# Kernel optimization log

Hardware: AMD Instinct MI355X
Metric: run time of the kernel (lower is better)

Reference implementation:

```python
import jax, jax.numpy as jnp
import numpy as np

EPS = 1e-9  # Dice BatchNormalization epsilon


def dice(x, alpha):
    # Keras BatchNormalization(axis=-1, center=False, scale=False) in training
    # mode: normalize over all axes except the last using batch statistics.
    mean = jnp.mean(x, axis=(0, 1), keepdims=True)
    var = jnp.var(x, axis=(0, 1), keepdims=True)
    x_normed = (x - mean) * jax.lax.rsqrt(var + EPS)
    p = jax.nn.sigmoid(x_normed)
    return alpha * (1.0 - p) * x + p * x


def setup_inputs() -> dict:
    key = jax.random.key(0)
    ks = jax.random.split(key, 11)
    B, T, D = 512, 2048, 20
    keys_ = jax.random.normal(ks[0], (B, T, D), dtype=jnp.float32)
    query = jax.random.normal(ks[1], (B, 1, D), dtype=jnp.float32)
    mask = jax.random.randint(ks[2], (B, T), 0, 2) > 0
    # DNN tower weights: hidden dims 80 -> 32 -> 16, attention head 16 -> 1
    W0 = jax.random.normal(ks[3], (80, 32), dtype=jnp.float32) * 0.1
    b0 = jax.random.normal(ks[4], (32,), dtype=jnp.float32) * 0.1
    a0 = jax.random.normal(ks[5], (32,), dtype=jnp.float32) * 0.1
    W1 = jax.random.normal(ks[6], (32, 16), dtype=jnp.float32) * 0.1
    b1 = jax.random.normal(ks[7], (16,), dtype=jnp.float32) * 0.1
    a1 = jax.random.normal(ks[8], (16,), dtype=jnp.float32) * 0.1
    wk = jax.random.normal(ks[9], (16, 1), dtype=jnp.float32) * 0.1
    bk = jax.random.normal(ks[10], (1,), dtype=jnp.float32) * 0.1
    return {"keys": keys_, "query": query, "mask": mask,
            "W0": W0, "b0": b0, "a0": a0,
            "W1": W1, "b1": b1, "a1": a1,
            "wk": wk, "bk": bk}


def reference(keys, query, mask, W0, b0, a0, W1, b1, a1, wk, bk):
    B, T, D = keys.shape
    # repeat query along the key/time axis: [B,1,D] -> [B,T,D]
    queries = jnp.broadcast_to(query, (B, T, D))
    # local-activation features: [B,T,4D] = [B,T,80]
    att = jnp.concatenate([queries, keys, queries - keys, queries * keys], axis=-1)
    # DNN tower with Dice activations (dropout is identity at inference)
    h = dice(att @ W0 + b0, a0)   # [B,T,32]
    h = dice(h @ W1 + b1, a1)     # [B,T,16]
    score = h @ wk + bk           # [B,T,1]
    outputs = jnp.transpose(score, (0, 2, 1))  # [B,1,T]
    # NOTE: the original code computes the masked scores into self.outputs but
    # then (weight_normalization=False, return_score=False) overwrites it with
    # matmul(outputs, keys) using the UNMASKED scores -- we reproduce that.
    return jnp.matmul(outputs, keys)  # [B,1,D]
```

## Files before the change

kernel.cpp:

```cpp
#include <hip/hip_runtime.h>
#include <hip/hip_cooperative_groups.h>

namespace cg = cooperative_groups;


#define BB 512
#define TT 2048
#define DD 20
#define C0 32
#define C1 16

#define NTH 256
#define NPOS 2
#define POSB (NTH * NPOS)
#define CHUNK 1024
#define NROUND (CHUNK / POSB)
#define NBLK (TT / CHUNK)
#define GRID (BB * NBLK)
#define NSLOT 8

#define WS_P1 0
#define WS_P2 512
#define WS_ZERO_N 768
#define WS_BLOB 896
#define BLOB_J 24
#define BLOB_B (C0 * BLOB_J)

#define PIN(x) asm volatile("" : "+v"(x))
#define AGLOAD(p) \
    __hip_atomic_load((p), __ATOMIC_RELAXED, __HIP_MEMORY_SCOPE_AGENT)

__device__ __forceinline__ float fast_sigmoid(float x) {
    return __builtin_amdgcn_rcpf(1.0f + __expf(-x));
}

__device__ __forceinline__ void load_krow(const float* __restrict__ row,
                                          float* kk) {
    const float4* kr = (const float4*)row;
    float4 a = kr[0], b = kr[1], c = kr[2], d = kr[3], e = kr[4];
    kk[0] = a.x; kk[1] = a.y; kk[2] = a.z; kk[3] = a.w;
    kk[4] = b.x; kk[5] = b.y; kk[6] = b.z; kk[7] = b.w;
    kk[8] = c.x; kk[9] = c.y; kk[10] = c.z; kk[11] = c.w;
    kk[12] = d.x; kk[13] = d.y; kk[14] = d.z; kk[15] = d.w;
    kk[16] = e.x; kk[17] = e.y; kk[18] = e.z; kk[19] = e.w;
}

__global__ void prep_kernel(const float* __restrict__ query,
                            const float* __restrict__ W0,
                            const float* __restrict__ b0,
                            float* __restrict__ blob, float* __restrict__ ws,
                            float* __restrict__ out) {
    const int b = blockIdx.x * 2 + (threadIdx.x >> 5);
    const int j = threadIdx.x & 31;
    if (blockIdx.x == 0) {
        for (int i = threadIdx.x; i < WS_ZERO_N; i += 64) ws[i] = 0.f;
    }
    if (j < DD) out[b * DD + j] = 0.f;
    float cj = b0[j];
    float* dst = blob + (size_t)b * BLOB_B + j * BLOB_J;
#pragma unroll
    for (int d = 0; d < DD; ++d) {
        float w_q = W0[d * C0 + j];
        float w_k = W0[(DD + d) * C0 + j];
        float w_d = W0[(2 * DD + d) * C0 + j];
        float w_p = W0[(3 * DD + d) * C0 + j];
        float qd = query[b * DD + d];
        dst[d] = w_k - w_d + qd * w_p;
        cj = fmaf(qd, w_q + w_d, cj);
    }
    dst[20] = cj;
}

#define LOAD_AND_PIN_KEYS(r)                                                 \
    float kk[NPOS][DD];                                                      \
    _Pragma("unroll") for (int pp = 0; pp < NPOS; ++pp)                      \
        load_krow(kbase + (size_t)((r)*POSB + tid + pp * NTH) * DD, kk[pp]); \
    _Pragma("unroll") for (int pp = 0; pp < NPOS; ++pp)                      \
        _Pragma("unroll") for (int d = 0; d < DD; ++d) PIN(kk[pp][d]);

#define TOWER_JLOOP()                                                        \
    _Pragma("unroll 1") for (int j = 0; j < C0; ++j) {                       \
        const float* wr = bA + j * BLOB_J;                                   \
        const float* ur = W1 + j * C1;                                       \
        const float cj = wr[20];                                             \
        const float2 ss = lss0[j];                                           \
        const float al = a0[j];                                              \
        const float nal = 1.0f - al;                                         \
        float h[NPOS];                                                       \
        _Pragma("unroll") for (int pp = 0; pp < NPOS; ++pp) {                \
            float hh = cj;                                                   \
            _Pragma("unroll") for (int d = 0; d < DD; ++d)                   \
                hh = fmaf(kk[pp][d], wr[d], hh);                             \
            h[pp] = hh;                                                      \
        }                                                                    \
        _Pragma("unroll") for (int pp = 0; pp < NPOS; ++pp) {                \
            float pr = fast_sigmoid(fmaf(h[pp], ss.x, ss.y));                \
            float h0d = h[pp] * fmaf(pr, nal, al);                           \
            _Pragma("unroll") for (int c = 0; c < C1; ++c)                   \
                h1[pp][c] = fmaf(h0d, ur[c], h1[pp][c]);                     \
        }                                                                    \
    }

__device__ __forceinline__ void phase1_body(int slot, int tid, int lane,
                                            const float* __restrict__ bA,
                                            const float* __restrict__ kbase,
                                            float* __restrict__ ws) {
    float s[C0], q[C0];
#pragma unroll
    for (int j = 0; j < C0; ++j) { s[j] = 0.f; q[j] = 0.f; }
#pragma unroll 1
    for (int r = 0; r < NROUND; ++r) {
        LOAD_AND_PIN_KEYS(r)
#pragma unroll
        for (int j = 0; j < C0; ++j) {
            const float* wr = bA + j * BLOB_J;
            const float cj = wr[20];
            float sv = 0.f, qv = 0.f;
#pragma unroll
            for (int pp = 0; pp < NPOS; ++pp) {
                float hh = cj;
#pragma unroll
                for (int d = 0; d < DD; ++d) hh = fmaf(kk[pp][d], wr[d], hh);
                sv += hh;
                qv = fmaf(hh, hh, qv);
            }
            s[j] += sv;
            q[j] += qv;
        }
    }
    float redv = 0.f;
#pragma unroll
    for (int v = 0; v < 2 * C0; ++v) {
        float val = (v < C0) ? s[v] : q[v - C0];
#pragma unroll
        for (int o = 32; o >= 1; o >>= 1) val += __shfl_xor(val, o);
        if (lane == v) redv = val;
    }
    atomicAdd(&ws[WS_P1 + slot * (2 * C0) + lane], redv);
}

__device__ __forceinline__ void finalize0(int tid, float* __restrict__ ws,
                                          float2* __restrict__ lss0) {
    if (tid < C0) {
        float sv = 0.f, qv = 0.f;
#pragma unroll
        for (int k = 0; k < NSLOT; ++k) {
            sv += AGLOAD(&ws[WS_P1 + k * (2 * C0) + tid]);
            qv += AGLOAD(&ws[WS_P1 + k * (2 * C0) + C0 + tid]);
        }
        const float invN = 1.0f / (float)(BB * TT);
        float mean = sv * invN;
        float var = qv * invN - mean * mean;
        float sc = rsqrtf(var + 1e-9f);
        lss0[tid] = make_float2(sc, -mean * sc);
    }
}

__device__ __forceinline__ void phase2_body(
    int slot, int tid, int lane, const float* __restrict__ bA,
    const float* __restrict__ kbase, const float* __restrict__ a0,
    const float* __restrict__ W1, const float* __restrict__ b1,
    const float2* __restrict__ lss0, float* __restrict__ ws) {
    float s1[C1], q1[C1];
#pragma unroll
    for (int c = 0; c < C1; ++c) { s1[c] = 0.f; q1[c] = 0.f; }
#pragma unroll 1
    for (int r = 0; r < NROUND; ++r) {
        LOAD_AND_PIN_KEYS(r)
        float h1[NPOS][C1];
#pragma unroll
        for (int pp = 0; pp < NPOS; ++pp)
#pragma unroll
            for (int c = 0; c < C1; ++c) h1[pp][c] = 0.f;
        TOWER_JLOOP()
#pragma unroll
        for (int c = 0; c < C1; ++c) {
            float bc = b1[c];
#pragma unroll
            for (int pp = 0; pp < NPOS; ++pp) {
                float v = h1[pp][c] + bc;
                s1[c] += v;
                q1[c] = fmaf(v, v, q1[c]);
            }
        }
    }
    float redv = 0.f;
#pragma unroll
    for (int v = 0; v < 2 * C1; ++v) {
        float val = (v < C1) ? s1[v] : q1[v - C1];
#pragma unroll
        for (int o = 32; o >= 1; o >>= 1) val += __shfl_xor(val, o);
        if (lane == v) redv = val;
    }
    if (lane < 2 * C1)
        atomicAdd(&ws[WS_P2 + slot * (2 * C1) + lane], redv);
}

__device__ __forceinline__ void finalize1(int tid, float* __restrict__ ws,
                                          const float* __restrict__ a1,
                                          const float* __restrict__ wk,
                                          float4* __restrict__ ld1v) {
    if (tid < C1) {
        float sv = 0.f, qv = 0.f;
#pragma unroll
        for (int k = 0; k < NSLOT; ++k) {
            sv += AGLOAD(&ws[WS_P2 + k * (2 * C1) + tid]);
            qv += AGLOAD(&ws[WS_P2 + k * (2 * C1) + C1 + tid]);
        }
        const float invN = 1.0f / (float)(BB * TT);
        float mean = sv * invN;
        float var = qv * invN - mean * mean;
        float sc = rsqrtf(var + 1e-9f);
        ld1v[tid] = make_float4(sc, -mean * sc, a1[tid], wk[tid]);
    }
}

__device__ __forceinline__ void phase3_body(
    int batch, int tid, int lane, int wave, const float* __restrict__ bA,
    const float* __restrict__ kbase, const float* __restrict__ a0,
    const float* __restrict__ W1, const float* __restrict__ b1,
    const float* __restrict__ bk, const float2* __restrict__ lss0,
    const float4* __restrict__ ld1v, float (*red)[DD],
    float* __restrict__ out) {
    const float bkv = bk[0];
    float oacc[DD];
#pragma unroll
    for (int d = 0; d < DD; ++d) oacc[d] = 0.f;
#pragma unroll 1
    for (int r = 0; r < NROUND; ++r) {
        LOAD_AND_PIN_KEYS(r)
        float h1[NPOS][C1];
#pragma unroll
        for (int pp = 0; pp < NPOS; ++pp)
#pragma unroll
            for (int c = 0; c < C1; ++c) h1[pp][c] = 0.f;
        TOWER_JLOOP()
#pragma unroll
        for (int pp = 0; pp < NPOS; ++pp) {
            float score = bkv;
#pragma unroll
            for (int c = 0; c < C1; ++c) {
                float v = h1[pp][c] + b1[c];
                float4 dv = ld1v[c];
                float pr = fast_sigmoid(fmaf(v, dv.x, dv.y));
                float hd = v * fmaf(pr, 1.0f - dv.z, dv.z);
                score = fmaf(hd, dv.w, score);
            }
#pragma unroll
            for (int d = 0; d < DD; ++d)
                oacc[d] = fmaf(score, kk[pp][d], oacc[d]);
        }
    }
    float redv = 0.f;
#pragma unroll
    for (int v = 0; v < DD; ++v) {
        float val = oacc[v];
#pragma unroll
        for (int o = 32; o >= 1; o >>= 1) val += __shfl_xor(val, o);
        if (lane == v) redv = val;
    }
    if (lane < DD) red[wave][lane] = redv;
    __syncthreads();
    if (tid < DD)
        atomicAdd(&out[batch * DD + tid],
                  red[0][tid] + red[1][tid] + red[2][tid] + red[3][tid]);
}

__global__ __launch_bounds__(NTH, 2) void fused_kernel(
    const float* __restrict__ keys, const float* __restrict__ blob,
    const float* __restrict__ a0, const float* __restrict__ W1,
    const float* __restrict__ b1, const float* __restrict__ a1,
    const float* __restrict__ wk, const float* __restrict__ bk,
    float* __restrict__ ws, float* __restrict__ out) {
    const int batch = blockIdx.x >> 1, chunk = blockIdx.x & 1;
    const int slot = blockIdx.x & (NSLOT - 1);
    const int tid = threadIdx.x, wave = tid >> 6, lane = tid & 63;
    const float* bA = blob + (size_t)batch * BLOB_B;
    const float* kbase = keys + ((size_t)batch * TT + chunk * CHUNK) * DD;

    __shared__ float2 lss0[C0];
    __shared__ float4 ld1v[C1];
    __shared__ float red[4][DD];

    phase1_body(slot, tid, lane, bA, kbase, ws);
    cg::this_grid().sync();
    finalize0(tid, ws, lss0);
    __syncthreads();
    phase2_body(slot, tid, lane, bA, kbase, a0, W1, b1, lss0, ws);
    cg::this_grid().sync();
    finalize1(tid, ws, a1, wk, ld1v);
    __syncthreads();
    phase3_body(batch, tid, lane, wave, bA, kbase, a0, W1, b1, bk, lss0,
                ld1v, red, out);
}

__global__ __launch_bounds__(NTH, 2) void pass1_kernel(
    const float* __restrict__ keys, const float* __restrict__ blob,
    float* __restrict__ ws) {
    const int batch = blockIdx.x >> 1, chunk = blockIdx.x & 1;
    const int tid = threadIdx.x, lane = tid & 63;
    phase1_body(blockIdx.x & (NSLOT - 1), tid, lane,
                blob + (size_t)batch * BLOB_B,
                keys + ((size_t)batch * TT + chunk * CHUNK) * DD, ws);
}

__global__ __launch_bounds__(NTH, 2) void pass2_kernel(
    const float* __restrict__ keys, const float* __restrict__ blob,
    const float* __restrict__ a0, const float* __restrict__ W1,
    const float* __restrict__ b1, float* __restrict__ ws) {
    const int batch = blockIdx.x >> 1, chunk = blockIdx.x & 1;
    const int tid = threadIdx.x, lane = tid & 63;
    __shared__ float2 lss0[C0];
    finalize0(tid, ws, lss0);
    __syncthreads();
    phase2_body(blockIdx.x & (NSLOT - 1), tid, lane,
                blob + (size_t)batch * BLOB_B,
                keys + ((size_t)batch * TT + chunk * CHUNK) * DD, a0, W1, b1,
                lss0, ws);
}

__global__ __launch_bounds__(NTH, 2) void pass3_kernel(
    const float* __restrict__ keys, const float* __restrict__ blob,
    const float* __restrict__ a0, const float* __restrict__ W1,
    const float* __restrict__ b1, const float* __restrict__ a1,
    const float* __restrict__ wk, const float* __restrict__ bk,
    float* __restrict__ ws, float* __restrict__ out) {
    const int batch = blockIdx.x >> 1, chunk = blockIdx.x & 1;
    const int tid = threadIdx.x, wave = tid >> 6, lane = tid & 63;
    __shared__ float2 lss0[C0];
    __shared__ float4 ld1v[C1];
    __shared__ float red[4][DD];
    finalize0(tid, ws, lss0);
    finalize1(tid, ws, a1, wk, ld1v);
    __syncthreads();
    phase3_body(batch, tid, lane, wave, blob + (size_t)batch * BLOB_B,
                keys + ((size_t)batch * TT + chunk * CHUNK) * DD, a0, W1, b1,
                bk, lss0, ld1v, red, out);
}

extern "C" void kernel_launch(void* const* d_in, const int* in_sizes, int n_in,
                              void* d_out, int out_size, void* d_ws,
                              size_t ws_size, hipStream_t stream) {
    const float* keys = (const float*)d_in[0];
    const float* query = (const float*)d_in[1];
    const float* W0 = (const float*)d_in[3];
    const float* b0 = (const float*)d_in[4];
    const float* a0 = (const float*)d_in[5];
    const float* W1 = (const float*)d_in[6];
    const float* b1 = (const float*)d_in[7];
    const float* a1 = (const float*)d_in[8];
    const float* wk = (const float*)d_in[9];
    const float* bk = (const float*)d_in[10];
    float* out = (float*)d_out;
    float* ws = (float*)d_ws;
    float* blob = ws + WS_BLOB;
    const float* blobc = blob;

    prep_kernel<<<BB / 2, 64, 0, stream>>>(query, W0, b0, blob, ws, out);

    static int use_coop = -1;
    if (use_coop < 0) {
        int nb = 0, ncu = 0;
        hipError_t e1 = hipOccupancyMaxActiveBlocksPerMultiprocessor(
            &nb, (const void*)fused_kernel, NTH, 0);
        hipDeviceProp_t prop;
        hipError_t e2 = hipGetDeviceProperties(&prop, 0);
        if (e2 == hipSuccess) ncu = prop.multiProcessorCount;
        use_coop = (e1 == hipSuccess && e2 == hipSuccess && nb * ncu >= GRID)
                       ? 1
                       : 0;
    }

    if (use_coop) {
        void* args[] = {(void*)&keys, (void*)&blobc, (void*)&a0, (void*)&W1,
                        (void*)&b1,   (void*)&a1,    (void*)&wk, (void*)&bk,
                        (void*)&ws,   (void*)&out};
        hipError_t e = hipLaunchCooperativeKernel(
            (const void*)fused_kernel, dim3(GRID), dim3(NTH), args, 0,
            stream);
        if (e != hipSuccess) use_coop = 0;
    }
    if (!use_coop) {
        pass1_kernel<<<GRID, NTH, 0, stream>>>(keys, blob, ws);
        pass2_kernel<<<GRID, NTH, 0, stream>>>(keys, blob, a0, W1, b1, ws);
        pass3_kernel<<<GRID, NTH, 0, stream>>>(keys, blob, a0, W1, b1, a1, wk,
                                               bk, ws, out);
    }
}
```

Baseline: 277.0 us.

## Stage key tiles through LDS with async double buffering, drop cooperative fused kernel

```diff
diff --git a/kernel.cpp b/kernel.cpp
--- a/kernel.cpp
+++ b/kernel.cpp
@@ -1,7 +1,4 @@
 #include <hip/hip_runtime.h>
-#include <hip/hip_cooperative_groups.h>
-
-namespace cg = cooperative_groups;
 
 
 #define BB 512
@@ -11,10 +8,9 @@
 #define C1 16
 
 #define NTH 256
-#define NPOS 2
-#define POSB (NTH * NPOS)
+#define TILE 256
 #define CHUNK 1024
-#define NROUND (CHUNK / POSB)
+#define SPB (CHUNK / TILE)
 #define NBLK (TT / CHUNK)
 #define GRID (BB * NBLK)
 #define NSLOT 8
@@ -30,14 +26,28 @@
 #define AGLOAD(p) \
     __hip_atomic_load((p), __ATOMIC_RELAXED, __HIP_MEMORY_SCOPE_AGENT)
 
+#define GAS __attribute__((address_space(1)))
+#define LAS __attribute__((address_space(3)))
+
 __device__ __forceinline__ float fast_sigmoid(float x) {
     return __builtin_amdgcn_rcpf(1.0f + __expf(-x));
 }
 
-__device__ __forceinline__ void load_krow(const float* __restrict__ row,
-                                          float* kk) {
-    const float4* kr = (const float4*)row;
-    float4 a = kr[0], b = kr[1], c = kr[2], d = kr[3], e = kr[4];
+__device__ __forceinline__ void stage_tile(const float* __restrict__ gsrc,
+                                           float* lbuf, int wave, int lane) {
+    const float* gw = gsrc + wave * 1280 + lane * 4;
+    float* lw_ = lbuf + wave * 1280;
+#pragma unroll
+    for (int u = 0; u < 5; ++u)
+        __builtin_amdgcn_global_load_lds((const GAS void*)(gw + u * 256),
+                                         (LAS void*)(lw_ + u * 256), 16, 0,
+                                         0);
+}
+
+__device__ __forceinline__ void load_row_lds(const float* __restrict__ row,
+                                             float* kk) {
+    const float4* r4 = (const float4*)row;
+    float4 a = r4[0], b = r4[1], c = r4[2], d = r4[3], e = r4[4];
     kk[0] = a.x; kk[1] = a.y; kk[2] = a.z; kk[3] = a.w;
     kk[4] = b.x; kk[5] = b.y; kk[6] = b.z; kk[7] = b.w;
     kk[8] = c.x; kk[9] = c.y; kk[10] = c.z; kk[11] = c.w;
@@ -71,74 +81,6 @@
     dst[20] = cj;
 }
 
-#define LOAD_AND_PIN_KEYS(r)                                                 \
-    float kk[NPOS][DD];                                                      \
-    _Pragma("unroll") for (int pp = 0; pp < NPOS; ++pp)                      \
-        load_krow(kbase + (size_t)((r)*POSB + tid + pp * NTH) * DD, kk[pp]); \
-    _Pragma("unroll") for (int pp = 0; pp < NPOS; ++pp)                      \
-        _Pragma("unroll") for (int d = 0; d < DD; ++d) PIN(kk[pp][d]);
-
-#define TOWER_JLOOP()                                                        \
-    _Pragma("unroll 1") for (int j = 0; j < C0; ++j) {                       \
-        const float* wr = bA + j * BLOB_J;                                   \
-        const float* ur = W1 + j * C1;                                       \
-        const float cj = wr[20];                                             \
-        const float2 ss = lss0[j];                                           \
-        const float al = a0[j];                                              \
-        const float nal = 1.0f - al;                                         \
-        float h[NPOS];                                                       \
-        _Pragma("unroll") for (int pp = 0; pp < NPOS; ++pp) {                \
-            float hh = cj;                                                   \
-            _Pragma("unroll") for (int d = 0; d < DD; ++d)                   \
-                hh = fmaf(kk[pp][d], wr[d], hh);                             \
-            h[pp] = hh;                                                      \
-        }                                                                    \
-        _Pragma("unroll") for (int pp = 0; pp < NPOS; ++pp) {                \
-            float pr = fast_sigmoid(fmaf(h[pp], ss.x, ss.y));                \
-            float h0d = h[pp] * fmaf(pr, nal, al);                           \
-            _Pragma("unroll") for (int c = 0; c < C1; ++c)                   \
-                h1[pp][c] = fmaf(h0d, ur[c], h1[pp][c]);                     \
-        }                                                                    \
-    }
-
-__device__ __forceinline__ void phase1_body(int slot, int tid, int lane,
-                                            const float* __restrict__ bA,
-                                            const float* __restrict__ kbase,
-                                            float* __restrict__ ws) {
-    float s[C0], q[C0];
-#pragma unroll
-    for (int j = 0; j < C0; ++j) { s[j] = 0.f; q[j] = 0.f; }
-#pragma unroll 1
-    for (int r = 0; r < NROUND; ++r) {
-        LOAD_AND_PIN_KEYS(r)
-#pragma unroll
-        for (int j = 0; j < C0; ++j) {
-            const float* wr = bA + j * BLOB_J;
-            const float cj = wr[20];
-            float sv = 0.f, qv = 0.f;
-#pragma unroll
-            for (int pp = 0; pp < NPOS; ++pp) {
-                float hh = cj;
-#pragma unroll
-                for (int d = 0; d < DD; ++d) hh = fmaf(kk[pp][d], wr[d], hh);
-                sv += hh;
-                qv = fmaf(hh, hh, qv);
-            }
-            s[j] += sv;
-            q[j] += qv;
-        }
-    }
-    float redv = 0.f;
-#pragma unroll
-    for (int v = 0; v < 2 * C0; ++v) {
-        float val = (v < C0) ? s[v] : q[v - C0];
-#pragma unroll
-        for (int o = 32; o >= 1; o >>= 1) val += __shfl_xor(val, o);
-        if (lane == v) redv = val;
-    }
-    atomicAdd(&ws[WS_P1 + slot * (2 * C0) + lane], redv);
-}
-
 __device__ __forceinline__ void finalize0(int tid, float* __restrict__ ws,
                                           float2* __restrict__ lss0) {
     if (tid < C0) {
@@ -154,46 +96,6 @@
         float sc = rsqrtf(var + 1e-9f);
         lss0[tid] = make_float2(sc, -mean * sc);
     }
-}
-
-__device__ __forceinline__ void phase2_body(
-    int slot, int tid, int lane, const float* __restrict__ bA,
-    const float* __restrict__ kbase, const float* __restrict__ a0,
-    const float* __restrict__ W1, const float* __restrict__ b1,
-    const float2* __restrict__ lss0, float* __restrict__ ws) {
-    float s1[C1], q1[C1];
-#pragma unroll
-    for (int c = 0; c < C1; ++c) { s1[c] = 0.f; q1[c] = 0.f; }
-#pragma unroll 1
-    for (int r = 0; r < NROUND; ++r) {
-        LOAD_AND_PIN_KEYS(r)
-        float h1[NPOS][C1];
-#pragma unroll
-        for (int pp = 0; pp < NPOS; ++pp)
-#pragma unroll
-            for (int c = 0; c < C1; ++c) h1[pp][c] = 0.f;
-        TOWER_JLOOP()
-#pragma unroll
-        for (int c = 0; c < C1; ++c) {
-            float bc = b1[c];
-#pragma unroll
-            for (int pp = 0; pp < NPOS; ++pp) {
-                float v = h1[pp][c] + bc;
-                s1[c] += v;
-                q1[c] = fmaf(v, v, q1[c]);
-            }
-        }
-    }
-    float redv = 0.f;
-#pragma unroll
-    for (int v = 0; v < 2 * C1; ++v) {
-        float val = (v < C1) ? s1[v] : q1[v - C1];
-#pragma unroll
-        for (int o = 32; o >= 1; o >>= 1) val += __shfl_xor(val, o);
-        if (lane == v) redv = val;
-    }
-    if (lane < 2 * C1)
-        atomicAdd(&ws[WS_P2 + slot * (2 * C1) + lane], redv);
 }
 
 __device__ __forceinline__ void finalize1(int tid, float* __restrict__ ws,
@@ -215,93 +117,53 @@
     }
 }
 
-__device__ __forceinline__ void phase3_body(
-    int batch, int tid, int lane, int wave, const float* __restrict__ bA,
-    const float* __restrict__ kbase, const float* __restrict__ a0,
-    const float* __restrict__ W1, const float* __restrict__ b1,
-    const float* __restrict__ bk, const float2* __restrict__ lss0,
-    const float4* __restrict__ ld1v, float (*red)[DD],
-    float* __restrict__ out) {
-    const float bkv = bk[0];
-    float oacc[DD];
-#pragma unroll
-    for (int d = 0; d < DD; ++d) oacc[d] = 0.f;
-#pragma unroll 1
-    for (int r = 0; r < NROUND; ++r) {
-        LOAD_AND_PIN_KEYS(r)
-        float h1[NPOS][C1];
-#pragma unroll
-        for (int pp = 0; pp < NPOS; ++pp)
-#pragma unroll
-            for (int c = 0; c < C1; ++c) h1[pp][c] = 0.f;
-        TOWER_JLOOP()
-#pragma unroll
-        for (int pp = 0; pp < NPOS; ++pp) {
-            float score = bkv;
-#pragma unroll
-            for (int c = 0; c < C1; ++c) {
-                float v = h1[pp][c] + b1[c];
-                float4 dv = ld1v[c];
-                float pr = fast_sigmoid(fmaf(v, dv.x, dv.y));
-                float hd = v * fmaf(pr, 1.0f - dv.z, dv.z);
-                score = fmaf(hd, dv.w, score);
-            }
-#pragma unroll
-            for (int d = 0; d < DD; ++d)
-                oacc[d] = fmaf(score, kk[pp][d], oacc[d]);
-        }
-    }
-    float redv = 0.f;
-#pragma unroll
-    for (int v = 0; v < DD; ++v) {
-        float val = oacc[v];
-#pragma unroll
-        for (int o = 32; o >= 1; o >>= 1) val += __shfl_xor(val, o);
-        if (lane == v) redv = val;
-    }
-    if (lane < DD) red[wave][lane] = redv;
-    __syncthreads();
-    if (tid < DD)
-        atomicAdd(&out[batch * DD + tid],
-                  red[0][tid] + red[1][tid] + red[2][tid] + red[3][tid]);
-}
-
-__global__ __launch_bounds__(NTH, 2) void fused_kernel(
+__global__ __launch_bounds__(NTH, 2) void pass1_kernel(
     const float* __restrict__ keys, const float* __restrict__ blob,
-    const float* __restrict__ a0, const float* __restrict__ W1,
-    const float* __restrict__ b1, const float* __restrict__ a1,
-    const float* __restrict__ wk, const float* __restrict__ bk,
-    float* __restrict__ ws, float* __restrict__ out) {
+    float* __restrict__ ws) {
     const int batch = blockIdx.x >> 1, chunk = blockIdx.x & 1;
     const int slot = blockIdx.x & (NSLOT - 1);
     const int tid = threadIdx.x, wave = tid >> 6, lane = tid & 63;
     const float* bA = blob + (size_t)batch * BLOB_B;
     const float* kbase = keys + ((size_t)batch * TT + chunk * CHUNK) * DD;
 
-    __shared__ float2 lss0[C0];
-    __shared__ float4 ld1v[C1];
-    __shared__ float red[4][DD];
-
-    phase1_body(slot, tid, lane, bA, kbase, ws);
-    cg::this_grid().sync();
-    finalize0(tid, ws, lss0);
+    __shared__ __align__(16) float kbuf[2][TILE * DD];
+
+    float s[C0], q[C0];
+#pragma unroll
+    for (int j = 0; j < C0; ++j) { s[j] = 0.f; q[j] = 0.f; }
+
+    stage_tile(kbase, kbuf[0], wave, lane);
     __syncthreads();
-    phase2_body(slot, tid, lane, bA, kbase, a0, W1, b1, lss0, ws);
-    cg::this_grid().sync();
-    finalize1(tid, ws, a1, wk, ld1v);
-    __syncthreads();
-    phase3_body(batch, tid, lane, wave, bA, kbase, a0, W1, b1, bk, lss0,
-                ld1v, red, out);
-}
-
-__global__ __launch_bounds__(NTH, 2) void pass1_kernel(
-    const float* __restrict__ keys, const float* __restrict__ blob,
-    float* __restrict__ ws) {
-    const int batch = blockIdx.x >> 1, chunk = blockIdx.x & 1;
-    const int tid = threadIdx.x, lane = tid & 63;
-    phase1_body(blockIdx.x & (NSLOT - 1), tid, lane,
-                blob + (size_t)batch * BLOB_B,
-                keys + ((size_t)batch * TT + chunk * CHUNK) * DD, ws);
+#pragma unroll 1
+    for (int st = 0; st < SPB; ++st) {
+        const int buf = st & 1;
+        if (st + 1 < SPB)
+            stage_tile(kbase + (size_t)(st + 1) * TILE * DD, kbuf[buf ^ 1],
+                       wave, lane);
+        float kk[DD];
+        load_row_lds(&kbuf[buf][tid * DD], kk);
+#pragma unroll
+        for (int d = 0; d < DD; ++d) PIN(kk[d]);
+#pragma unroll
+        for (int j = 0; j < C0; ++j) {
+            const float* wr = bA + j * BLOB_J;
+            float hh = wr[20];
+#pragma unroll
+            for (int d = 0; d < DD; ++d) hh = fmaf(kk[d], wr[d], hh);
+            s[j] += hh;
+            q[j] = fmaf(hh, hh, q[j]);
+        }
+        __syncthreads();
+    }
+    float redv = 0.f;
+#pragma unroll
+    for (int v = 0; v < 2 * C0; ++v) {
+        float val = (v < C0) ? s[v] : q[v - C0];
+#pragma unroll
+        for (int o = 32; o >= 1; o >>= 1) val += __shfl_xor(val, o);
+        if (lane == v) redv = val;
+    }
+    atomicAdd(&ws[WS_P1 + slot * (2 * C0) + lane], redv);
 }
 
 __global__ __launch_bounds__(NTH, 2) void pass2_kernel(
@@ -309,14 +171,67 @@
     const float* __restrict__ a0, const float* __restrict__ W1,
     const float* __restrict__ b1, float* __restrict__ ws) {
     const int batch = blockIdx.x >> 1, chunk = blockIdx.x & 1;
-    const int tid = threadIdx.x, lane = tid & 63;
+    const int slot = blockIdx.x & (NSLOT - 1);
+    const int tid = threadIdx.x, wave = tid >> 6, lane = tid & 63;
+    const float* bA = blob + (size_t)batch * BLOB_B;
+    const float* kbase = keys + ((size_t)batch * TT + chunk * CHUNK) * DD;
+
+    __shared__ __align__(16) float kbuf[2][TILE * DD];
     __shared__ float2 lss0[C0];
+
     finalize0(tid, ws, lss0);
+
+    float s1[C1], q1[C1];
+#pragma unroll
+    for (int c = 0; c < C1; ++c) { s1[c] = 0.f; q1[c] = 0.f; }
+
+    stage_tile(kbase, kbuf[0], wave, lane);
     __syncthreads();
-    phase2_body(blockIdx.x & (NSLOT - 1), tid, lane,
-                blob + (size_t)batch * BLOB_B,
-                keys + ((size_t)batch * TT + chunk * CHUNK) * DD, a0, W1, b1,
-                lss0, ws);
+#pragma unroll 1
+    for (int st = 0; st < SPB; ++st) {
+        const int buf = st & 1;
+        if (st + 1 < SPB)
+            stage_tile(kbase + (size_t)(st + 1) * TILE * DD, kbuf[buf ^ 1],
+                       wave, lane);
+        float kk[DD];
+        load_row_lds(&kbuf[buf][tid * DD], kk);
+#pragma unroll
+        for (int d = 0; d < DD; ++d) PIN(kk[d]);
+        float h1[C1];
+#pragma unroll
+        for (int c = 0; c < C1; ++c) h1[c] = 0.f;
+#pragma unroll
+        for (int j = 0; j < C0; ++j) {
+            const float* wr = bA + j * BLOB_J;
+            const float* ur = W1 + j * C1;
+            const float2 ss = lss0[j];
+            const float al = a0[j];
+            float hh = wr[20];
+#pragma unroll
+            for (int d = 0; d < DD; ++d) hh = fmaf(kk[d], wr[d], hh);
+            float pr = fast_sigmoid(fmaf(hh, ss.x, ss.y));
+            float h0d = hh * fmaf(pr, 1.0f - al, al);
+#pragma unroll
+            for (int c = 0; c < C1; ++c) h1[c] = fmaf(h0d, ur[c], h1[c]);
+        }
+#pragma unroll
+        for (int c = 0; c < C1; ++c) {
+            float v = h1[c] + b1[c];
+            s1[c] += v;
+            q1[c] = fmaf(v, v, q1[c]);
+        }
+        __syncthreads();
+    }
+    float redv = 0.f;
+#pragma unroll
+    for (int v = 0; v < 2 * C1; ++v) {
+        float val = (v < C1) ? s1[v] : q1[v - C1];
+#pragma unroll
+        for (int o = 32; o >= 1; o >>= 1) val += __shfl_xor(val, o);
+        if (lane == v) redv = val;
+    }
+    if (lane < 2 * C1)
+        atomicAdd(&ws[WS_P2 + slot * (2 * C1) + lane], redv);
 }
 
 __global__ __launch_bounds__(NTH, 2) void pass3_kernel(
@@ -327,15 +242,77 @@
     float* __restrict__ ws, float* __restrict__ out) {
     const int batch = blockIdx.x >> 1, chunk = blockIdx.x & 1;
     const int tid = threadIdx.x, wave = tid >> 6, lane = tid & 63;
+    const float* bA = blob + (size_t)batch * BLOB_B;
+    const float* kbase = keys + ((size_t)batch * TT + chunk * CHUNK) * DD;
+
+    __shared__ __align__(16) float kbuf[2][TILE * DD];
     __shared__ float2 lss0[C0];
     __shared__ float4 ld1v[C1];
     __shared__ float red[4][DD];
+
     finalize0(tid, ws, lss0);
     finalize1(tid, ws, a1, wk, ld1v);
+
+    const float bkv = bk[0];
+    float oacc[DD];
+#pragma unroll
+    for (int d = 0; d < DD; ++d) oacc[d] = 0.f;
+
+    stage_tile(kbase, kbuf[0], wave, lane);
     __syncthreads();
-    phase3_body(batch, tid, lane, wave, blob + (size_t)batch * BLOB_B,
-                keys + ((size_t)batch * TT + chunk * CHUNK) * DD, a0, W1, b1,
-                bk, lss0, ld1v, red, out);
+#pragma unroll 1
+    for (int st = 0; st < SPB; ++st) {
+        const int buf = st & 1;
+        if (st + 1 < SPB)
+            stage_tile(kbase + (size_t)(st + 1) * TILE * DD, kbuf[buf ^ 1],
+                       wave, lane);
+        float kk[DD];
+        load_row_lds(&kbuf[buf][tid * DD], kk);
+#pragma unroll
+        for (int d = 0; d < DD; ++d) PIN(kk[d]);
+        float h1[C1];
+#pragma unroll
+        for (int c = 0; c < C1; ++c) h1[c] = 0.f;
+#pragma unroll
+        for (int j = 0; j < C0; ++j) {
+            const float* wr = bA + j * BLOB_J;
+            const float* ur = W1 + j * C1;
+            const float2 ss = lss0[j];
+            const float al = a0[j];
+            float hh = wr[20];
+#pragma unroll
+            for (int d = 0; d < DD; ++d) hh = fmaf(kk[d], wr[d], hh);
+            float pr = fast_sigmoid(fmaf(hh, ss.x, ss.y));
+            float h0d = hh * fmaf(pr, 1.0f - al, al);
+#pragma unroll
+            for (int c = 0; c < C1; ++c) h1[c] = fmaf(h0d, ur[c], h1[c]);
+        }
+        float score = bkv;
+#pragma unroll
+        for (int c = 0; c < C1; ++c) {
+            float v = h1[c] + b1[c];
+            float4 dv = ld1v[c];
+            float pr = fast_sigmoid(fmaf(v, dv.x, dv.y));
+            float hd = v * fmaf(pr, 1.0f - dv.z, dv.z);
+            score = fmaf(hd, dv.w, score);
+        }
+#pragma unroll
+        for (int d = 0; d < DD; ++d) oacc[d] = fmaf(score, kk[d], oacc[d]);
+        __syncthreads();
+    }
+    float redv = 0.f;
+#pragma unroll
+    for (int v = 0; v < DD; ++v) {
+        float val = oacc[v];
+#pragma unroll
+        for (int o = 32; o >= 1; o >>= 1) val += __shfl_xor(val, o);
+        if (lane == v) redv = val;
+    }
+    if (lane < DD) red[wave][lane] = redv;
+    __syncthreads();
+    if (tid < DD)
+        atomicAdd(&out[batch * DD + tid],
+                  red[0][tid] + red[1][tid] + red[2][tid] + red[3][tid]);
 }
 
 extern "C" void kernel_launch(void* const* d_in, const int* in_sizes, int n_in,
@@ -354,36 +331,10 @@
     float* out = (float*)d_out;
     float* ws = (float*)d_ws;
     float* blob = ws + WS_BLOB;
-    const float* blobc = blob;
 
     prep_kernel<<<BB / 2, 64, 0, stream>>>(query, W0, b0, blob, ws, out);
-
-    static int use_coop = -1;
-    if (use_coop < 0) {
-        int nb = 0, ncu = 0;
-        hipError_t e1 = hipOccupancyMaxActiveBlocksPerMultiprocessor(
-            &nb, (const void*)fused_kernel, NTH, 0);
-        hipDeviceProp_t prop;
-        hipError_t e2 = hipGetDeviceProperties(&prop, 0);
-        if (e2 == hipSuccess) ncu = prop.multiProcessorCount;
-        use_coop = (e1 == hipSuccess && e2 == hipSuccess && nb * ncu >= GRID)
-                       ? 1
-                       : 0;
-    }
-
-    if (use_coop) {
-        void* args[] = {(void*)&keys, (void*)&blobc, (void*)&a0, (void*)&W1,
-                        (void*)&b1,   (void*)&a1,    (void*)&wk, (void*)&bk,
-                        (void*)&ws,   (void*)&out};
-        hipError_t e = hipLaunchCooperativeKernel(
-            (const void*)fused_kernel, dim3(GRID), dim3(NTH), args, 0,
-            stream);
-        if (e != hipSuccess) use_coop = 0;
-    }
-    if (!use_coop) {
-        pass1_kernel<<<GRID, NTH, 0, stream>>>(keys, blob, ws);
-        pass2_kernel<<<GRID, NTH, 0, stream>>>(keys, blob, a0, W1, b1, ws);
-        pass3_kernel<<<GRID, NTH, 0, stream>>>(keys, blob, a0, W1, b1, a1, wk,
-                                               bk, ws, out);
-    }
-}
+    pass1_kernel<<<GRID, NTH, 0, stream>>>(keys, blob, ws);
+    pass2_kernel<<<GRID, NTH, 0, stream>>>(keys, blob, a0, W1, b1, ws);
+    pass3_kernel<<<GRID, NTH, 0, stream>>>(keys, blob, a0, W1, b1, a1, wk,
+                                           bk, ws, out);
+}
```

New measurement: 319.6 us. 1.15x slower.
